# Kernel tuning notes

Hardware: AMD Instinct MI355X
Metric: run time of the kernel (lower is better)

Reference implementation:

```python
import jax, jax.numpy as jnp
import numpy as np

N = 50000   # nodes
E = 600000  # edges (avg degree 12)
D = 128     # embedding_dim == hidden_features
L = 4       # depth


def setup_inputs() -> dict:
    key = jax.random.key(0)
    k0, k1, k2, k3 = jax.random.split(key, 4)
    scale = 1.0 / np.sqrt(D)
    node_embedding = jax.random.normal(k0, (N, D), jnp.float32)
    edge_index = jax.random.randint(k1, (2, E), 0, N, dtype=jnp.int32)
    Ws_rel = jax.random.normal(k2, (L, D, D), jnp.float32) * scale
    bs_rel = jnp.zeros((L, D), jnp.float32)
    Ws_root = jax.random.normal(k3, (L, D, D), jnp.float32) * scale
    return {
        'node_embedding': node_embedding,
        'edge_index': edge_index,
        'Ws_rel': Ws_rel,
        'bs_rel': bs_rel,
        'Ws_root': Ws_root,
    }


def reference(node_embedding, edge_index, Ws_rel, bs_rel, Ws_root):
    # PyG GraphConv (aggr='mean'), flow source_to_target:
    #   out_i = lin_rel(mean_{j in N(i)} x_j) + lin_root(x_i)
    # followed by ELU (dropout probs are 0 -> identity).
    n = node_embedding.shape[0]
    src, dst = edge_index[0], edge_index[1]
    ones = jnp.ones((edge_index.shape[1],), node_embedding.dtype)
    deg = jax.ops.segment_sum(ones, dst, num_segments=n)
    inv_deg = (1.0 / jnp.maximum(deg, 1.0))[:, None]  # [n, 1]
    X = node_embedding
    for l in range(Ws_rel.shape[0]):
        agg = jax.ops.segment_sum(X[src], dst, num_segments=n) * inv_deg  # [n, D]
        out = agg @ Ws_rel[l] + bs_rel[l] + X @ Ws_root[l]
        X = jax.nn.elu(out)
    return X
```

## Files before the change

kernel.cpp:

```cpp
#include <hip/hip_runtime.h>

#define D 128
#define LDR 264
#define SLOTS 64
#define EPB 2048

typedef short bf16x8 __attribute__((ext_vector_type(8)));
typedef float f32x4 __attribute__((ext_vector_type(4)));

__device__ __forceinline__ unsigned short f2bf(float f) {
  unsigned int u = __float_as_uint(f);
  unsigned int r = (u + 0x7fff + ((u >> 16) & 1)) >> 16;
  return (unsigned short)r;
}
__device__ __forceinline__ unsigned int pack2bf(float lo, float hi) {
  return (unsigned int)f2bf(lo) | ((unsigned int)f2bf(hi) << 16);
}

__global__ __launch_bounds__(256) void k_build(
    const int* __restrict__ src, const int* __restrict__ dst, int E, int N,
    int* __restrict__ cursor, unsigned short* __restrict__ csr64,
    const float* __restrict__ X0, unsigned short* __restrict__ Xb, int total4,
    const float* __restrict__ Wrel, const float* __restrict__ Wroot,
    unsigned short* __restrict__ Wp, int wtot,
    int fb, int cb) {
  int b = blockIdx.x;
  if (b < fb) {
    int p = b & 7;
    int chunk = b >> 3;
    int lo = (int)((long long)p * N / 8);
    int hi = (int)((long long)(p + 1) * N / 8);
    int base = chunk * EPB + threadIdx.x;
#pragma unroll
    for (int it = 0; it < EPB / 256; ++it, base += 256) {
      if (base < E) {
        int d = dst[base];
        if (d >= lo && d < hi) {
          int ps = atomicAdd(&cursor[d], 1);
          if (ps < SLOTS) csr64[d * SLOTS + ps] = (unsigned short)src[base];
        }
      }
    }
    return;
  }
  b -= fb;
  if (b < cb) {
    int i = b * 256 + threadIdx.x;
    if (i < total4) {
      float4 v = ((const float4*)X0)[i];
      ushort4 o;
      o.x = f2bf(v.x); o.y = f2bf(v.y); o.z = f2bf(v.z); o.w = f2bf(v.w);
      ((ushort4*)Xb)[i] = o;
    }
    return;
  }
  b -= cb;
  {
    int gid = b * 256 + threadIdx.x;
    if (gid >= wtot) return;
    int lane = gid & 63;
    int t = gid >> 6;
    int ctg = t & 7; t >>= 3;
    int ks = t & 7; t >>= 3;
    int l = t;
    const float* Wr = Wrel + (size_t)l * D * D;
    const float* Wo = Wroot + (size_t)l * D * D;
    int colc = ctg * 16 + (lane & 15);
    int krow0 = ks * 32 + (lane >> 4) * 8;
    unsigned short tmp[8];
#pragma unroll
    for (int j = 0; j < 8; ++j) {
      int kr = krow0 + j;
      float w = (kr < D) ? Wr[(size_t)kr * D + colc] : Wo[(size_t)(kr - D) * D + colc];
      tmp[j] = f2bf(w);
    }
    unsigned short* dstp = Wp + ((size_t)gid) * 8;
#pragma unroll
    for (int j = 0; j < 8; ++j) dstp[j] = tmp[j];
  }
}


#define ACC8(v) \
    acc[0] += __uint_as_float((v).x << 16); acc[1] += __uint_as_float((v).x & 0xffff0000u); \
    acc[2] += __uint_as_float((v).y << 16); acc[3] += __uint_as_float((v).y & 0xffff0000u); \
    acc[4] += __uint_as_float((v).z << 16); acc[5] += __uint_as_float((v).z & 0xffff0000u); \
    acc[6] += __uint_as_float((v).w << 16); acc[7] += __uint_as_float((v).w & 0xffff0000u);

__global__ __launch_bounds__(256, 4) void k_layer_fused(
    const unsigned short* __restrict__ Xin,
    const int* __restrict__ cursor, const unsigned short* __restrict__ csr64,
    const unsigned short* __restrict__ Wp_l, const float* __restrict__ bias,
    unsigned short* __restrict__ Xnext, float* __restrict__ out_f32,
    int last, int N) {
  __shared__ __align__(16) unsigned short sRow[64 * LDR];
  int tid = threadIdx.x;
  int r0 = blockIdx.x * 64;
  int wave = tid >> 6, lane = tid & 63;
  int grp = lane >> 4;
  int l16 = lane & 15;

  for (int i = tid; i < 64 * 16; i += 256) {
    int r = i >> 4, c = i & 15;
    int row = r0 + r;
    uint4 v = make_uint4(0u, 0u, 0u, 0u);
    if (row < N) v = *(const uint4*)(Xin + (size_t)row * D + c * 8);
    *(uint4*)(&sRow[r * LDR + (16 + c) * 8]) = v;
  }

  int node0 = r0 + wave * 16;
  int deg_n = 0, eid_n = 0;
  if (node0 < N) {
    deg_n = cursor[node0];
    eid_n = (int)csr64[(size_t)node0 * SLOTS + lane];
  }
  for (int k = 0; k < 16; ++k) {
    int curnode = node0 + k;
    int deg = deg_n;
    int eid = eid_n;
    int nxt = curnode + 1;
    if (k < 15 && nxt < N) {
      deg_n = cursor[nxt];
      eid_n = (int)csr64[(size_t)nxt * SLOTS + lane];
    } else {
      deg_n = 0; eid_n = 0;
    }

    float acc[8];
#pragma unroll
    for (int t = 0; t < 8; ++t) acc[t] = 0.f;

    if (curnode < N) {
      int n = min(deg, SLOTS);
      int j4 = 0;
      for (; j4 + 12 <= n; j4 += 12) {
        int s0 = __shfl(eid, j4 + grp);
        int s1 = __shfl(eid, j4 + 4 + grp);
        int s2 = __shfl(eid, j4 + 8 + grp);
        uint4 v0 = *(const uint4*)(Xin + (size_t)s0 * D + l16 * 8);
        uint4 v1 = *(const uint4*)(Xin + (size_t)s1 * D + l16 * 8);
        uint4 v2 = *(const uint4*)(Xin + (size_t)s2 * D + l16 * 8);
        ACC8(v0) ACC8(v1) ACC8(v2)
      }
      if (j4 + 8 <= n) {
        int s0 = __shfl(eid, j4 + grp);
        int s1 = __shfl(eid, j4 + 4 + grp);
        uint4 v0 = *(const uint4*)(Xin + (size_t)s0 * D + l16 * 8);
        uint4 v1 = *(const uint4*)(Xin + (size_t)s1 * D + l16 * 8);
        ACC8(v0) ACC8(v1)
        j4 += 8;
      }
      for (; j4 < n; j4 += 4) {
        int jj = j4 + grp;
        int s = __shfl(eid, jj);
        if (jj < n) {
          uint4 v = *(const uint4*)(Xin + (size_t)s * D + l16 * 8);
          ACC8(v)
        }
      }
#pragma unroll
      for (int t = 0; t < 8; ++t) {
        acc[t] += __shfl_xor(acc[t], 16);
        acc[t] += __shfl_xor(acc[t], 32);
      }
    }

    if (grp == 0) {
      float inv = 1.0f / fmaxf((float)deg, 1.0f);
      uint4 o;
      o.x = pack2bf(acc[0] * inv, acc[1] * inv);
      o.y = pack2bf(acc[2] * inv, acc[3] * inv);
      o.z = pack2bf(acc[4] * inv, acc[5] * inv);
      o.w = pack2bf(acc[6] * inv, acc[7] * inv);
      *(uint4*)(&sRow[(wave * 16 + k) * LDR + l16 * 8]) = o;
    }
  }
  __syncthreads();

  int m = l16, q = grp;
  int ct0 = wave * 2;

  f32x4 cacc[4][2];
#pragma unroll
  for (int g = 0; g < 4; ++g)
#pragma unroll
    for (int c = 0; c < 2; ++c) cacc[g][c] = (f32x4){0.f, 0.f, 0.f, 0.f};

  const unsigned short* arow = &sRow[m * LDR + q * 8];
#pragma unroll
  for (int ks = 0; ks < 8; ++ks) {
    bf16x8 b0 = *(const bf16x8*)(Wp_l + ((size_t)((ks * 8 + ct0 + 0) * 64 + lane)) * 8);
    bf16x8 b1 = *(const bf16x8*)(Wp_l + ((size_t)((ks * 8 + ct0 + 1) * 64 + lane)) * 8);
    bf16x8 a0 = *(const bf16x8*)(arow + ks * 32);
    bf16x8 a1 = *(const bf16x8*)(arow + 16 * LDR + ks * 32);
    bf16x8 a2 = *(const bf16x8*)(arow + 32 * LDR + ks * 32);
    bf16x8 a3 = *(const bf16x8*)(arow + 48 * LDR + ks * 32);
    cacc[0][0] = __builtin_amdgcn_mfma_f32_16x16x32_bf16(a0, b0, cacc[0][0], 0, 0, 0);
    cacc[0][1] = __builtin_amdgcn_mfma_f32_16x16x32_bf16(a0, b1, cacc[0][1], 0, 0, 0);
    cacc[1][0] = __builtin_amdgcn_mfma_f32_16x16x32_bf16(a1, b0, cacc[1][0], 0, 0, 0);
    cacc[1][1] = __builtin_amdgcn_mfma_f32_16x16x32_bf16(a1, b1, cacc[1][1], 0, 0, 0);
    cacc[2][0] = __builtin_amdgcn_mfma_f32_16x16x32_bf16(a2, b0, cacc[2][0], 0, 0, 0);
    cacc[2][1] = __builtin_amdgcn_mfma_f32_16x16x32_bf16(a2, b1, cacc[2][1], 0, 0, 0);
    cacc[3][0] = __builtin_amdgcn_mfma_f32_16x16x32_bf16(a3, b0, cacc[3][0], 0, 0, 0);
    cacc[3][1] = __builtin_amdgcn_mfma_f32_16x16x32_bf16(a3, b1, cacc[3][1], 0, 0, 0);
  }

#pragma unroll
  for (int g = 0; g < 4; ++g) {
#pragma unroll
    for (int c = 0; c < 2; ++c) {
      int col = (ct0 + c) * 16 + m;
      float bv = bias[col];
      int rbase = r0 + g * 16 + q * 4;
#pragma unroll
      for (int j = 0; j < 4; ++j) {
        int row = rbase + j;
        float v = cacc[g][c][j] + bv;
        float e = __expf(fminf(v, 0.f)) - 1.f;
        v = v > 0.f ? v : e;
        if (last) {
          if (row < N) out_f32[(size_t)row * D + col] = v;
        } else {
          unsigned int h = (unsigned int)f2bf(v);
          unsigned int nb = (unsigned int)__shfl_xor((int)h, 1);
          if (!(m & 1) && row < N)
            *(unsigned int*)(Xnext + (size_t)row * D + col) = h | (nb << 16);
        }
      }
    }
  }
}


extern "C" void kernel_launch(void* const* d_in, const int* in_sizes, int n_in,
                              void* d_out, int out_size, void* d_ws, size_t ws_size,
                              hipStream_t stream) {
  const float* X0    = (const float*)d_in[0];
  const int*   eidx  = (const int*)d_in[1];
  const float* Wrel  = (const float*)d_in[2];
  const float* brel  = (const float*)d_in[3];
  const float* Wroot = (const float*)d_in[4];
  float* out = (float*)d_out;

  const int N = in_sizes[0] / D;
  const int E = in_sizes[1] / 2;
  const int L = in_sizes[3] / D;
  const int* src = eidx;
  const int* dst = eidx + E;

  char* ws = (char*)d_ws;
  size_t off = 0;
  auto carve = [&](size_t bytes) -> void* {
    void* p = ws + off;
    off = (off + bytes + 255) & ~(size_t)255;
    return p;
  };
  unsigned short* Xb0  = (unsigned short*)carve((size_t)N * D * sizeof(unsigned short));
  unsigned short* Xb1  = (unsigned short*)carve((size_t)N * D * sizeof(unsigned short));
  unsigned short* Wp   = (unsigned short*)carve((size_t)L * 4096 * 8 * sizeof(unsigned short));
  int*            cursor = (int*)carve((size_t)N * sizeof(int));
  unsigned short* csr64  = (unsigned short*)carve((size_t)N * SLOTS * sizeof(unsigned short));
  (void)ws_size; (void)n_in; (void)out_size;

  hipMemsetAsync(cursor, 0, (size_t)N * sizeof(int), stream);

  const int chunks = (E + EPB - 1) / EPB;
  const int fb = chunks * 8;
  const int total4 = N * D / 4;
  const int cb = (total4 + 255) / 256;
  const int wtot = L * 4096;
  const int wb = (wtot + 255) / 256;
  k_build<<<fb + cb + wb, 256, 0, stream>>>(src, dst, E, N, cursor, csr64,
      X0, Xb0, total4, Wrel, Wroot, Wp, wtot, fb, cb);

  const int lb = (N + 63) / 64;

  const unsigned short* Xcur = Xb0;
  for (int l = 0; l < L; ++l) {
    int last = (l == L - 1) ? 1 : 0;
    unsigned short* Xnext = (Xcur == Xb0) ? Xb1 : Xb0;
    k_layer_fused<<<lb, 256, 0, stream>>>(Xcur, cursor, csr64,
        Wp + (size_t)l * 4096 * 8, brel + (size_t)l * D, Xnext, out, last, N);
    Xcur = Xnext;
  }
}
```

Baseline: 283.9 us.

## Assign one node per 16-lane group in gather instead of one node per wave

The neighbor-mean gather is restructured so each 16-lane quarter-wave handles its own node (four nodes per wave at a time) instead of the whole wave splitting one node's edges four ways and reducing with cross-lane shuffles. Edge ids, degrees and root rows for all four slots are loaded up front, and each group issues eight independent row loads per step before accumulating. This removes the cross-group xor reductions and gives more memory loads in flight. In exchange it adds more registers, diverges when nodes in a wave have uneven degrees, and makes some loads to row 0 for padded edges.

```diff
diff --git a/kernel.cpp b/kernel.cpp
--- a/kernel.cpp
+++ b/kernel.cpp
@@ -100,80 +100,60 @@
   int grp = lane >> 4;
   int l16 = lane & 15;
 
-  for (int i = tid; i < 64 * 16; i += 256) {
-    int r = i >> 4, c = i & 15;
-    int row = r0 + r;
-    uint4 v = make_uint4(0u, 0u, 0u, 0u);
-    if (row < N) v = *(const uint4*)(Xin + (size_t)row * D + c * 8);
-    *(uint4*)(&sRow[r * LDR + (16 + c) * 8]) = v;
-  }
-
-  int node0 = r0 + wave * 16;
-  int deg_n = 0, eid_n = 0;
-  if (node0 < N) {
-    deg_n = cursor[node0];
-    eid_n = (int)csr64[(size_t)node0 * SLOTS + lane];
-  }
-  for (int k = 0; k < 16; ++k) {
-    int curnode = node0 + k;
-    int deg = deg_n;
-    int eid = eid_n;
-    int nxt = curnode + 1;
-    if (k < 15 && nxt < N) {
-      deg_n = cursor[nxt];
-      eid_n = (int)csr64[(size_t)nxt * SLOTS + lane];
-    } else {
-      deg_n = 0; eid_n = 0;
-    }
+  int deg[4];
+  uint2 bkt[4];
+  uint4 vroot[4];
+#pragma unroll
+  for (int s = 0; s < 4; ++s) {
+    int node = r0 + wave * 16 + s * 4 + grp;
+    bool val = node < N;
+    deg[s] = val ? cursor[node] : 0;
+    bkt[s] = val ? *(const uint2*)(csr64 + (size_t)node * SLOTS + l16 * 4)
+                 : make_uint2(0u, 0u);
+    vroot[s] = val ? *(const uint4*)(Xin + (size_t)node * D + l16 * 8)
+                   : make_uint4(0u, 0u, 0u, 0u);
+  }
+
+#pragma unroll
+  for (int s = 0; s < 4; ++s) {
+    int r = wave * 16 + s * 4 + grp;
+    *(uint4*)(&sRow[r * LDR + (16 + l16) * 8]) = vroot[s];
 
     float acc[8];
 #pragma unroll
     for (int t = 0; t < 8; ++t) acc[t] = 0.f;
 
-    if (curnode < N) {
-      int n = min(deg, SLOTS);
-      int j4 = 0;
-      for (; j4 + 12 <= n; j4 += 12) {
-        int s0 = __shfl(eid, j4 + grp);
-        int s1 = __shfl(eid, j4 + 4 + grp);
-        int s2 = __shfl(eid, j4 + 8 + grp);
-        uint4 v0 = *(const uint4*)(Xin + (size_t)s0 * D + l16 * 8);
-        uint4 v1 = *(const uint4*)(Xin + (size_t)s1 * D + l16 * 8);
-        uint4 v2 = *(const uint4*)(Xin + (size_t)s2 * D + l16 * 8);
-        ACC8(v0) ACC8(v1) ACC8(v2)
-      }
-      if (j4 + 8 <= n) {
-        int s0 = __shfl(eid, j4 + grp);
-        int s1 = __shfl(eid, j4 + 4 + grp);
-        uint4 v0 = *(const uint4*)(Xin + (size_t)s0 * D + l16 * 8);
-        uint4 v1 = *(const uint4*)(Xin + (size_t)s1 * D + l16 * 8);
-        ACC8(v0) ACC8(v1)
-        j4 += 8;
-      }
-      for (; j4 < n; j4 += 4) {
-        int jj = j4 + grp;
-        int s = __shfl(eid, jj);
-        if (jj < n) {
-          uint4 v = *(const uint4*)(Xin + (size_t)s * D + l16 * 8);
-          ACC8(v)
-        }
-      }
+    int n = min(deg[s], SLOTS);
+    for (int j = 0; j < n; j += 8) {
+      int a = grp * 16 + (j >> 2);
+      unsigned ua_x = (unsigned)__shfl((int)bkt[s].x, a);
+      unsigned ua_y = (unsigned)__shfl((int)bkt[s].y, a);
+      unsigned ub_x = (unsigned)__shfl((int)bkt[s].x, a + 1);
+      unsigned ub_y = (unsigned)__shfl((int)bkt[s].y, a + 1);
+      int e[8];
+      e[0] = (int)(ua_x & 0xffffu); e[1] = (int)(ua_x >> 16);
+      e[2] = (int)(ua_y & 0xffffu); e[3] = (int)(ua_y >> 16);
+      e[4] = (int)(ub_x & 0xffffu); e[5] = (int)(ub_x >> 16);
+      e[6] = (int)(ub_y & 0xffffu); e[7] = (int)(ub_y >> 16);
+      uint4 vv[8];
 #pragma unroll
       for (int t = 0; t < 8; ++t) {
-        acc[t] += __shfl_xor(acc[t], 16);
-        acc[t] += __shfl_xor(acc[t], 32);
-      }
-    }
-
-    if (grp == 0) {
-      float inv = 1.0f / fmaxf((float)deg, 1.0f);
-      uint4 o;
-      o.x = pack2bf(acc[0] * inv, acc[1] * inv);
-      o.y = pack2bf(acc[2] * inv, acc[3] * inv);
-      o.z = pack2bf(acc[4] * inv, acc[5] * inv);
-      o.w = pack2bf(acc[6] * inv, acc[7] * inv);
-      *(uint4*)(&sRow[(wave * 16 + k) * LDR + l16 * 8]) = o;
-    }
+        int idx = (j + t < n) ? e[t] : 0;
+        vv[t] = *(const uint4*)(Xin + (size_t)idx * D + l16 * 8);
+      }
+#pragma unroll
+      for (int t = 0; t < 8; ++t) {
+        if (j + t < n) { ACC8(vv[t]) }
+      }
+    }
+
+    float inv = 1.0f / fmaxf((float)deg[s], 1.0f);
+    uint4 o;
+    o.x = pack2bf(acc[0] * inv, acc[1] * inv);
+    o.y = pack2bf(acc[2] * inv, acc[3] * inv);
+    o.z = pack2bf(acc[4] * inv, acc[5] * inv);
+    o.w = pack2bf(acc[6] * inv, acc[7] * inv);
+    *(uint4*)(&sRow[r * LDR + l16 * 8]) = o;
   }
   __syncthreads();
 
```

Measured after the change: 243.4 us. -14.3%, faster.
